# Kernel optimization log

Hardware: AMD Instinct MI355X
Metric: run time of the kernel (lower is better)

The kernel has to match this reference:

```python
import jax, jax.numpy as jnp
import numpy as np
from jax import lax

H = 1024       # hidden_size
I = 1024       # intermediate_size (per expert)
E = 16         # num_experts
TOP_K = 4      # num_active_experts


def setup_inputs() -> dict:
    key = jax.random.key(0)
    ks = jax.random.split(key, 9)
    std_gate = 0.02 / (E ** 0.5)
    return {
        "hidden_states": jax.random.normal(ks[0], (1, 2048, H), jnp.float32),
        "gate_w": jax.random.normal(ks[1], (E, H), jnp.float32) * std_gate,
        "expert_bias": jnp.zeros((E,), jnp.float32),
        "w1": jax.random.normal(ks[2], (E, I, H), jnp.float32) * 0.02,
        "w2": jax.random.normal(ks[3], (E, H, I), jnp.float32) * 0.02,
        "w3": jax.random.normal(ks[4], (E, I, H), jnp.float32) * 0.02,
        "sw1": jax.random.normal(ks[5], (I, H), jnp.float32) * 0.02,
        "sw2": jax.random.normal(ks[6], (H, I), jnp.float32) * 0.02,
        "sw3": jax.random.normal(ks[7], (I, H), jnp.float32) * 0.02,
    }


def _swiglu(x, wg, wd, wu):
    # Swish(x W1^T) * (x W3^T) then W2^T
    return (jax.nn.silu(x @ wg.T) * (x @ wu.T)) @ wd.T


def reference(hidden_states, gate_w, expert_bias, w1, w2, w3, sw1, sw2, sw3):
    B, S, Hd = hidden_states.shape
    x = hidden_states.reshape(-1, Hd)              # [T, H]
    T = x.shape[0]

    # ---- Router ----
    router_logits = x @ gate_w.T                   # [T, E]
    biased = router_logits + expert_bias           # loss-free balancing bias
    _, sel = lax.top_k(biased, TOP_K)              # [T, K] indices from biased logits
    raw = jnp.take_along_axis(router_logits, sel, axis=-1)  # weights from UNbiased logits
    rw = jax.nn.softmax(raw.astype(jnp.float32), axis=-1).astype(x.dtype)  # [T, K]

    # Dense combine weights g[t, e] = routing weight if e selected else 0
    g = jnp.zeros((T, E), x.dtype).at[jnp.arange(T)[:, None], sel].add(rw)

    # ---- Routed experts (mathematically equal to grouped dispatch) ----
    routed = jnp.zeros_like(x)
    for e in range(E):  # fixed small expert loop
        routed = routed + g[:, e:e + 1] * _swiglu(x, w1[e], w2[e], w3[e])

    # ---- Shared expert ----
    shared = _swiglu(x, sw1, sw2, sw3)

    out = (shared + routed).reshape(B, S, Hd)      # dropout p=0 -> identity
    return out
```

## Files before the change

kernel.cpp:

```cpp
#include <hip/hip_runtime.h>
#include <cstddef>
#include <cstdint>

#define T_TOK 2048
#define HD 1024
#define ID 1024
#define NE 16
#define TOPK 4
#define BM 128
#define BN 128
#define BK 32
#define MT_MAX 96
#define SLOT_CAP (MT_MAX * BM)

typedef float f32x4 __attribute__((ext_vector_type(4)));
typedef __bf16 bf16x8 __attribute__((ext_vector_type(8)));
typedef __bf16 bf16x4 __attribute__((ext_vector_type(4)));

#define WS_TILE_E 256
#define WS_LOGITS 4096
#define WS_SLOT_TOK (WS_LOGITS + T_TOK * NE * 4)
#define WS_SLOT_W (WS_SLOT_TOK + SLOT_CAP * 4)
#define WS_H1 (WS_SLOT_W + SLOT_CAP * 4)
#define WS_XB (WS_H1 + (size_t)SLOT_CAP * ID * 2)
#define WS_W1B (WS_XB + (size_t)T_TOK * HD * 2)
#define WS_W2B (WS_W1B + (size_t)NE * ID * HD * 2)
#define WS_W3B (WS_W2B + (size_t)NE * HD * ID * 2)
#define WS_SW1B (WS_W3B + (size_t)NE * ID * HD * 2)
#define WS_SW2B (WS_SW1B + (size_t)ID * HD * 2)
#define WS_SW3B (WS_SW2B + (size_t)HD * ID * 2)
#define WS_NEED (WS_SW3B + (size_t)ID * HD * 2)

__device__ __forceinline__ f32x4 mfma16(bf16x8 a, bf16x8 b, f32x4 c) {
  return __builtin_amdgcn_mfma_f32_16x16x32_bf16(a, b, c, 0, 0, 0);
}

__device__ __forceinline__ bf16x4 pack4(f32x4 a) {
  bf16x4 o;
  o[0] = (__bf16)a[0]; o[1] = (__bf16)a[1]; o[2] = (__bf16)a[2]; o[3] = (__bf16)a[3];
  return o;
}

__device__ __forceinline__ void gload16(const __bf16* g, __bf16* l) {
  __builtin_amdgcn_global_load_lds(
      (const __attribute__((address_space(1))) uint32_t*)g,
      (__attribute__((address_space(3))) uint32_t*)l, 16, 0, 0);
}

#define W4 ((size_t)1 << 22)
#define S4 ((size_t)1 << 18)
#define X4 ((size_t)1 << 19)
#define CVT4_TOTAL (3 * W4 + 3 * S4 + X4)
#define NCHUNK (CVT4_TOTAL / 2048)
#define CVT_GRID 2048
#define LOGITS_BLOCKS (T_TOK / 4)

__global__ __launch_bounds__(256) void fused_pre(
    const float* __restrict__ w1, const float* __restrict__ w2,
    const float* __restrict__ w3, const float* __restrict__ sw1,
    const float* __restrict__ sw2, const float* __restrict__ sw3,
    const float* __restrict__ x, __bf16* __restrict__ w1b,
    __bf16* __restrict__ w2b, __bf16* __restrict__ w3b,
    __bf16* __restrict__ sw1b, __bf16* __restrict__ sw2b,
    __bf16* __restrict__ sw3b, __bf16* __restrict__ xb,
    const float* __restrict__ gw, float* __restrict__ logits) {
  int tid = threadIdx.x;
  if ((int)blockIdx.x < LOGITS_BLOCKS) {
    int wv = tid >> 6;
    int lane = tid & 63;
    int tok = blockIdx.x * 4 + wv;
    int e = lane >> 2;
    int q = lane & 3;
    const float4* xr = (const float4*)(x + (size_t)tok * HD) + q * 64;
    const float4* wr = (const float4*)(gw + (size_t)e * HD) + q * 64;
    float s0 = 0.f, s1 = 0.f;
#pragma unroll 8
    for (int i = 0; i < 64; i += 2) {
      float4 a0 = xr[i], w0 = wr[i];
      float4 a1 = xr[i + 1], w1v = wr[i + 1];
      s0 += a0.x * w0.x + a0.y * w0.y + a0.z * w0.z + a0.w * w0.w;
      s1 += a1.x * w1v.x + a1.y * w1v.y + a1.z * w1v.z + a1.w * w1v.w;
    }
    float s = s0 + s1;
    s += __shfl_xor(s, 1);
    s += __shfl_xor(s, 2);
    if (q == 0) logits[(size_t)tok * NE + e] = s;
    return;
  }
  size_t b = blockIdx.x - LOGITS_BLOCKS;
  for (size_t c = b; c < NCHUNK; c += CVT_GRID) {
    size_t f = c * 2048;
    const float* src;
    __bf16* dst;
    size_t off;
    if (f < 3 * W4) {
      size_t t = f >> 22;
      off = f & (W4 - 1);
      src = (t == 0) ? w1 : (t == 1) ? w2 : w3;
      dst = (t == 0) ? w1b : (t == 1) ? w2b : w3b;
    } else {
      size_t j = f - 3 * W4;
      if (j < 3 * S4) {
        size_t t = j >> 18;
        off = j & (S4 - 1);
        src = (t == 0) ? sw1 : (t == 1) ? sw2 : sw3;
        dst = (t == 0) ? sw1b : (t == 1) ? sw2b : sw3b;
      } else {
        off = j - 3 * S4;
        src = x;
        dst = xb;
      }
    }
    const f32x4* p = (const f32x4*)src + off + tid;
    __bf16* q = dst + 4 * (off + tid);
    f32x4 v0 = __builtin_nontemporal_load(p);
    f32x4 v1 = __builtin_nontemporal_load(p + 256);
    f32x4 v2 = __builtin_nontemporal_load(p + 512);
    f32x4 v3 = __builtin_nontemporal_load(p + 768);
    f32x4 v4 = __builtin_nontemporal_load(p + 1024);
    f32x4 v5 = __builtin_nontemporal_load(p + 1280);
    f32x4 v6 = __builtin_nontemporal_load(p + 1536);
    f32x4 v7 = __builtin_nontemporal_load(p + 1792);
    *(bf16x4*)(q + 0 * 1024) = pack4(v0);
    *(bf16x4*)(q + 1 * 1024) = pack4(v1);
    *(bf16x4*)(q + 2 * 1024) = pack4(v2);
    *(bf16x4*)(q + 3 * 1024) = pack4(v3);
    *(bf16x4*)(q + 4 * 1024) = pack4(v4);
    *(bf16x4*)(q + 5 * 1024) = pack4(v5);
    *(bf16x4*)(q + 6 * 1024) = pack4(v6);
    *(bf16x4*)(q + 7 * 1024) = pack4(v7);
  }
}

__global__ __launch_bounds__(256) void router_finish(
    const float* __restrict__ logits, const float* __restrict__ bias,
    int* __restrict__ tile_e, int* __restrict__ slot_tok,
    float* __restrict__ slot_w) {
  __shared__ int hist[NE];
  __shared__ int soff[NE + 1];
  __shared__ int fillp[NE];
  __shared__ unsigned lsel[T_TOK];
  __shared__ float4 lw4[T_TOK];

  int tid = threadIdx.x;
  if (tid < NE) { hist[tid] = 0; fillp[tid] = 0; }
  __syncthreads();

  float bb[NE];
#pragma unroll
  for (int e = 0; e < NE; ++e) bb[e] = bias[e];

  for (int j = 0; j < T_TOK / 256; ++j) {
    int t = tid + 256 * j;
    float lg[NE];
    const float4* lp = (const float4*)(logits + (size_t)t * NE);
#pragma unroll
    for (int q = 0; q < 4; ++q) {
      float4 v = lp[q];
      lg[4 * q] = v.x; lg[4 * q + 1] = v.y; lg[4 * q + 2] = v.z; lg[4 * q + 3] = v.w;
    }
    float b[NE];
#pragma unroll
    for (int e = 0; e < NE; ++e) b[e] = lg[e] + bb[e];

    int selk[TOPK];
    float raw[TOPK];
    unsigned used = 0;
#pragma unroll
    for (int k = 0; k < TOPK; ++k) {
      float best = -3.4e38f;
      int bi = 0;
#pragma unroll
      for (int e = 0; e < NE; ++e) {
        if (!((used >> e) & 1) && b[e] > best) { best = b[e]; bi = e; }
      }
      used |= (1u << bi);
      selk[k] = bi;
      raw[k] = lg[bi];
    }
    float m = raw[0];
#pragma unroll
    for (int k = 1; k < TOPK; ++k) m = fmaxf(m, raw[k]);
    float s = 0.f;
    float w[TOPK];
#pragma unroll
    for (int k = 0; k < TOPK; ++k) { w[k] = __expf(raw[k] - m); s += w[k]; }
    float inv = 1.f / s;
    lsel[t] = (unsigned)selk[0] | ((unsigned)selk[1] << 8) |
              ((unsigned)selk[2] << 16) | ((unsigned)selk[3] << 24);
    lw4[t] = make_float4(w[0] * inv, w[1] * inv, w[2] * inv, w[3] * inv);
#pragma unroll
    for (int k = 0; k < TOPK; ++k) atomicAdd(&hist[selk[k]], 1);
  }
  __syncthreads();

  if (tid == 0) {
    int o = 0;
    for (int e = 0; e < NE; ++e) { soff[e] = o; o += (hist[e] + BM - 1) & ~(BM - 1); }
    soff[NE] = o;
  }
  __syncthreads();
  int shared_base = soff[NE];
  int total = shared_base + T_TOK;
  for (int tt = tid; tt < MT_MAX; tt += 256) {
    int base = tt * BM;
    int ee = -1;
    if (base < shared_base) {
      ee = 0;
#pragma unroll
      for (int q = 1; q < NE; ++q) if (base >= soff[q]) ee = q;
    } else if (base < total) {
      ee = NE;
    }
    tile_e[tt] = ee;
  }

  for (int j = 0; j < T_TOK / 256; ++j) {
    int t = tid + 256 * j;
    unsigned ps = lsel[t];
    float4 wv = lw4[t];
    int e0 = ps & 255, e1 = (ps >> 8) & 255, e2 = (ps >> 16) & 255, e3 = ps >> 24;
    int p0 = atomicAdd(&fillp[e0], 1);
    slot_tok[soff[e0] + p0] = t; slot_w[soff[e0] + p0] = wv.x;
    int p1 = atomicAdd(&fillp[e1], 1);
    slot_tok[soff[e1] + p1] = t; slot_w[soff[e1] + p1] = wv.y;
    int p2 = atomicAdd(&fillp[e2], 1);
    slot_tok[soff[e2] + p2] = t; slot_w[soff[e2] + p2] = wv.z;
    int p3 = atomicAdd(&fillp[e3], 1);
    slot_tok[soff[e3] + p3] = t; slot_w[soff[e3] + p3] = wv.w;
  }

  for (int s = tid; s < shared_base; s += 256) {
    int e = 0;
#pragma unroll
    for (int q = 1; q < NE; ++q) if (s >= soff[q]) e = q;
    if (s >= soff[e] + hist[e]) { slot_tok[s] = -1; slot_w[s] = 0.f; }
  }
  for (int s = shared_base + tid; s < total; s += 256) {
    slot_tok[s] = s - shared_base;
    slot_w[s] = 1.0f;
  }
}


__global__ __launch_bounds__(256, 2) void pass1_bf16(
    const __bf16* __restrict__ xb, const int* __restrict__ slot_tok,
    const int* __restrict__ tile_e, const __bf16* __restrict__ w1b,
    const __bf16* __restrict__ w3b, const __bf16* __restrict__ sw1b,
    const __bf16* __restrict__ sw3b, __bf16* __restrict__ h1) {
  int mt = blockIdx.y;
  int e = tile_e[mt];
  if (e < 0) return;
  int n0 = blockIdx.x * BN;
  int m0 = mt * BM;

  const __bf16* wg = (e == NE) ? sw1b : w1b + (size_t)e * ID * HD;
  const __bf16* wu = (e == NE) ? sw3b : w3b + (size_t)e * ID * HD;

  __shared__ __align__(16) __bf16 As[2][BM * BK];
  __shared__ __align__(16) __bf16 Bg[2][BN * BK];
  __shared__ __align__(16) __bf16 Bu[2][BN * BK];

  int tid = threadIdx.x;
  int r0 = tid >> 2, r1 = r0 + 64;
  int c8 = ((tid & 3) ^ ((r0 >> 1) & 3)) * 8;
  int tok0 = slot_tok[m0 + r0]; if (tok0 < 0) tok0 = 0;
  int tok1 = slot_tok[m0 + r1]; if (tok1 < 0) tok1 = 0;
  const __bf16* gA0 = xb + (size_t)tok0 * HD + c8;
  const __bf16* gA1 = xb + (size_t)tok1 * HD + c8;
  const __bf16* gG0 = wg + (size_t)(n0 + r0) * HD + c8;
  const __bf16* gG1 = wg + (size_t)(n0 + r1) * HD + c8;
  const __bf16* gU0 = wu + (size_t)(n0 + r0) * HD + c8;
  const __bf16* gU1 = wu + (size_t)(n0 + r1) * HD + c8;

  int wave = tid >> 6, lane = tid & 63;
  int wm = (wave >> 1) * 64, wn = (wave & 1) * 64;
  int l16 = lane & 15, kch = lane >> 4;
  int kk8 = (kch ^ ((l16 >> 1) & 3)) * 8;

  f32x4 accg[4][4] = {};
  f32x4 accu[4][4] = {};

  auto stage = [&](int B, int k0) {
    gload16(gA0 + k0, &As[B][(size_t)tid * 8]);
    gload16(gA1 + k0, &As[B][(size_t)(tid + 256) * 8]);
    gload16(gG0 + k0, &Bg[B][(size_t)tid * 8]);
    gload16(gG1 + k0, &Bg[B][(size_t)(tid + 256) * 8]);
    gload16(gU0 + k0, &Bu[B][(size_t)tid * 8]);
    gload16(gU1 + k0, &Bu[B][(size_t)(tid + 256) * 8]);
  };
  auto body = [&](int B) {
    bf16x8 af[4], gf[4], uf[4];
#pragma unroll
    for (int i = 0; i < 4; ++i) {
      af[i] = *(const bf16x8*)(&As[B][(wm + i * 16 + l16) * BK + kk8]);
      gf[i] = *(const bf16x8*)(&Bg[B][(wn + i * 16 + l16) * BK + kk8]);
      uf[i] = *(const bf16x8*)(&Bu[B][(wn + i * 16 + l16) * BK + kk8]);
    }
    asm volatile("s_waitcnt lgkmcnt(0)" ::: "memory");
    __builtin_amdgcn_s_barrier();
    __builtin_amdgcn_sched_barrier(0);
#pragma unroll
    for (int mi = 0; mi < 4; ++mi)
#pragma unroll
      for (int ni = 0; ni < 4; ++ni) {
        accg[mi][ni] = mfma16(af[mi], gf[ni], accg[mi][ni]);
        accu[mi][ni] = mfma16(af[mi], uf[ni], accu[mi][ni]);
      }
  };

  stage(0, 0);
#pragma unroll 1
  for (int k = 0; k < HD / BK - 1; ++k) {
    int cur = k & 1;
    stage(cur ^ 1, (k + 1) * BK);
    asm volatile("s_waitcnt vmcnt(6)" ::: "memory");
    __builtin_amdgcn_s_barrier();
    __builtin_amdgcn_sched_barrier(0);
    body(cur);
  }
  asm volatile("s_waitcnt vmcnt(0)" ::: "memory");
  __builtin_amdgcn_s_barrier();
  __builtin_amdgcn_sched_barrier(0);
  body((HD / BK - 1) & 1);

#pragma unroll
  for (int mi = 0; mi < 4; ++mi) {
#pragma unroll
    for (int ni = 0; ni < 4; ++ni) {
#pragma unroll
      for (int j = 0; j < 4; ++j) {
        int row = m0 + wm + mi * 16 + kch * 4 + j;
        int col = n0 + wn + ni * 16 + l16;
        float g = accg[mi][ni][j];
        float u = accu[mi][ni][j];
        float hv = (g / (1.f + __expf(-g))) * u;
        h1[(size_t)row * ID + col] = (__bf16)hv;
      }
    }
  }
}

__global__ __launch_bounds__(256, 3) void pass2_bf16(
    const __bf16* __restrict__ h1, const int* __restrict__ slot_tok,
    const float* __restrict__ slot_w, const int* __restrict__ tile_e,
    const __bf16* __restrict__ w2b, const __bf16* __restrict__ sw2b,
    float* __restrict__ out) {
  int mt = blockIdx.y;
  int e = tile_e[mt];
  if (e < 0) return;
  int n0 = blockIdx.x * BN;
  int m0 = mt * BM;

  const __bf16* wd = (e == NE) ? sw2b : w2b + (size_t)e * HD * ID;

  __shared__ __align__(16) __bf16 As[2][BM * BK];
  __shared__ __align__(16) __bf16 Bs[2][BN * BK];

  int tid = threadIdx.x;
  int r0 = tid >> 2, r1 = r0 + 64;
  int c8 = ((tid & 3) ^ ((r0 >> 1) & 3)) * 8;
  const __bf16* gA0 = h1 + (size_t)(m0 + r0) * ID + c8;
  const __bf16* gA1 = h1 + (size_t)(m0 + r1) * ID + c8;
  const __bf16* gB0 = wd + (size_t)(n0 + r0) * ID + c8;
  const __bf16* gB1 = wd + (size_t)(n0 + r1) * ID + c8;

  int wave = tid >> 6, lane = tid & 63;
  int wm = (wave >> 1) * 64, wn = (wave & 1) * 64;
  int l16 = lane & 15, kch = lane >> 4;
  int kk8 = (kch ^ ((l16 >> 1) & 3)) * 8;

  f32x4 acc[4][4] = {};

  auto stage = [&](int B, int k0) {
    gload16(gA0 + k0, &As[B][(size_t)tid * 8]);
    gload16(gA1 + k0, &As[B][(size_t)(tid + 256) * 8]);
    gload16(gB0 + k0, &Bs[B][(size_t)tid * 8]);
    gload16(gB1 + k0, &Bs[B][(size_t)(tid + 256) * 8]);
  };
  auto body = [&](int B) {
    bf16x8 af[4], bf[4];
#pragma unroll
    for (int i = 0; i < 4; ++i) {
      af[i] = *(const bf16x8*)(&As[B][(wm + i * 16 + l16) * BK + kk8]);
      bf[i] = *(const bf16x8*)(&Bs[B][(wn + i * 16 + l16) * BK + kk8]);
    }
    asm volatile("s_waitcnt lgkmcnt(0)" ::: "memory");
    __builtin_amdgcn_s_barrier();
    __builtin_amdgcn_sched_barrier(0);
#pragma unroll
    for (int mi = 0; mi < 4; ++mi)
#pragma unroll
      for (int ni = 0; ni < 4; ++ni)
        acc[mi][ni] = mfma16(af[mi], bf[ni], acc[mi][ni]);
  };

  stage(0, 0);
#pragma unroll 1
  for (int k = 0; k < ID / BK - 1; ++k) {
    int cur = k & 1;
    stage(cur ^ 1, (k + 1) * BK);
    asm volatile("s_waitcnt vmcnt(4)" ::: "memory");
    __builtin_amdgcn_s_barrier();
    __builtin_amdgcn_sched_barrier(0);
    body(cur);
  }
  asm volatile("s_waitcnt vmcnt(0)" ::: "memory");
  __builtin_amdgcn_s_barrier();
  __builtin_amdgcn_sched_barrier(0);
  body((ID / BK - 1) & 1);

#pragma unroll
  for (int mi = 0; mi < 4; ++mi) {
#pragma unroll
    for (int j = 0; j < 4; ++j) {
      int row = m0 + wm + mi * 16 + kch * 4 + j;
      int token = slot_tok[row];
      if (token < 0) continue;
      float wgt = slot_w[row];
#pragma unroll
      for (int ni = 0; ni < 4; ++ni) {
        int col = n0 + wn + ni * 16 + l16;
        atomicAdd(out + (size_t)token * HD + col, wgt * acc[mi][ni][j]);
      }
    }
  }
}

extern "C" void kernel_launch(void* const* d_in, const int* in_sizes, int n_in,
                              void* d_out, int out_size, void* d_ws, size_t ws_size,
                              hipStream_t stream) {
  const float* x = (const float*)d_in[0];
  const float* gate_w = (const float*)d_in[1];
  const float* ebias = (const float*)d_in[2];
  const float* w1 = (const float*)d_in[3];
  const float* w2 = (const float*)d_in[4];
  const float* w3 = (const float*)d_in[5];
  const float* sw1 = (const float*)d_in[6];
  const float* sw2 = (const float*)d_in[7];
  const float* sw3 = (const float*)d_in[8];
  float* out = (float*)d_out;

  char* ws = (char*)d_ws;
  int* tile_e = (int*)(ws + WS_TILE_E);
  float* logits = (float*)(ws + WS_LOGITS);
  int* slot_tok = (int*)(ws + WS_SLOT_TOK);
  float* slot_w = (float*)(ws + WS_SLOT_W);
  __bf16* h1 = (__bf16*)(ws + WS_H1);
  __bf16* xb = (__bf16*)(ws + WS_XB);
  __bf16* w1b = (__bf16*)(ws + WS_W1B);
  __bf16* w2b = (__bf16*)(ws + WS_W2B);
  __bf16* w3b = (__bf16*)(ws + WS_W3B);
  __bf16* sw1b = (__bf16*)(ws + WS_SW1B);
  __bf16* sw2b = (__bf16*)(ws + WS_SW2B);
  __bf16* sw3b = (__bf16*)(ws + WS_SW3B);

  hipMemsetAsync(d_out, 0, (size_t)T_TOK * HD * sizeof(float), stream);

  fused_pre<<<LOGITS_BLOCKS + CVT_GRID, 256, 0, stream>>>(
      w1, w2, w3, sw1, sw2, sw3, x, w1b, w2b, w3b, sw1b, sw2b, sw3b, xb,
      gate_w, logits);
  router_finish<<<1, 256, 0, stream>>>(logits, ebias, tile_e, slot_tok, slot_w);

  pass1_bf16<<<dim3(ID / BN, MT_MAX), 256, 0, stream>>>(
      xb, slot_tok, tile_e, w1b, w3b, sw1b, sw3b, h1);
  pass2_bf16<<<dim3(HD / BN, MT_MAX), 256, 0, stream>>>(
      h1, slot_tok, slot_w, tile_e, w2b, sw2b, out);
}
```

Baseline: 242.0 us.

## Fuse fp32-to-bf16 weight conversion into GEMM tile loads

Drops the separate pass that converted all expert and shared weights to bf16 in workspace. The GEMMs now load fp32 weight tiles straight into LDS with a swizzled layout and convert to bf16 while reading fragments. This removes a full read-and-write of roughly 200MB of weights. In exchange each tile doubles its global and LDS traffic, and the conversion is repeated for every M tile that reuses an expert's weights. LDS use grows, which may lower occupancy.

```diff
diff --git a/kernel.cpp b/kernel.cpp
--- a/kernel.cpp
+++ b/kernel.cpp
@@ -23,16 +23,16 @@
 #define WS_SLOT_W (WS_SLOT_TOK + SLOT_CAP * 4)
 #define WS_H1 (WS_SLOT_W + SLOT_CAP * 4)
 #define WS_XB (WS_H1 + (size_t)SLOT_CAP * ID * 2)
-#define WS_W1B (WS_XB + (size_t)T_TOK * HD * 2)
-#define WS_W2B (WS_W1B + (size_t)NE * ID * HD * 2)
-#define WS_W3B (WS_W2B + (size_t)NE * HD * ID * 2)
-#define WS_SW1B (WS_W3B + (size_t)NE * ID * HD * 2)
-#define WS_SW2B (WS_SW1B + (size_t)ID * HD * 2)
-#define WS_SW3B (WS_SW2B + (size_t)HD * ID * 2)
-#define WS_NEED (WS_SW3B + (size_t)ID * HD * 2)
 
 __device__ __forceinline__ f32x4 mfma16(bf16x8 a, bf16x8 b, f32x4 c) {
   return __builtin_amdgcn_mfma_f32_16x16x32_bf16(a, b, c, 0, 0, 0);
+}
+
+__device__ __forceinline__ bf16x8 pack8(f32x4 a, f32x4 b) {
+  bf16x8 o;
+  o[0] = (__bf16)a[0]; o[1] = (__bf16)a[1]; o[2] = (__bf16)a[2]; o[3] = (__bf16)a[3];
+  o[4] = (__bf16)b[0]; o[5] = (__bf16)b[1]; o[6] = (__bf16)b[2]; o[7] = (__bf16)b[3];
+  return o;
 }
 
 __device__ __forceinline__ bf16x4 pack4(f32x4 a) {
@@ -46,24 +46,18 @@
       (const __attribute__((address_space(1))) uint32_t*)g,
       (__attribute__((address_space(3))) uint32_t*)l, 16, 0, 0);
 }
-
-#define W4 ((size_t)1 << 22)
-#define S4 ((size_t)1 << 18)
-#define X4 ((size_t)1 << 19)
-#define CVT4_TOTAL (3 * W4 + 3 * S4 + X4)
-#define NCHUNK (CVT4_TOTAL / 2048)
-#define CVT_GRID 2048
+__device__ __forceinline__ void gload16f(const float* g, float* l) {
+  __builtin_amdgcn_global_load_lds(
+      (const __attribute__((address_space(1))) uint32_t*)g,
+      (__attribute__((address_space(3))) uint32_t*)l, 16, 0, 0);
+}
+
 #define LOGITS_BLOCKS (T_TOK / 4)
+#define XCHUNKS 256
 
 __global__ __launch_bounds__(256) void fused_pre(
-    const float* __restrict__ w1, const float* __restrict__ w2,
-    const float* __restrict__ w3, const float* __restrict__ sw1,
-    const float* __restrict__ sw2, const float* __restrict__ sw3,
-    const float* __restrict__ x, __bf16* __restrict__ w1b,
-    __bf16* __restrict__ w2b, __bf16* __restrict__ w3b,
-    __bf16* __restrict__ sw1b, __bf16* __restrict__ sw2b,
-    __bf16* __restrict__ sw3b, __bf16* __restrict__ xb,
-    const float* __restrict__ gw, float* __restrict__ logits) {
+    const float* __restrict__ x, const float* __restrict__ gw,
+    __bf16* __restrict__ xb, float* __restrict__ logits) {
   int tid = threadIdx.x;
   if ((int)blockIdx.x < LOGITS_BLOCKS) {
     int wv = tid >> 6;
@@ -87,49 +81,19 @@
     if (q == 0) logits[(size_t)tok * NE + e] = s;
     return;
   }
-  size_t b = blockIdx.x - LOGITS_BLOCKS;
-  for (size_t c = b; c < NCHUNK; c += CVT_GRID) {
-    size_t f = c * 2048;
-    const float* src;
-    __bf16* dst;
-    size_t off;
-    if (f < 3 * W4) {
-      size_t t = f >> 22;
-      off = f & (W4 - 1);
-      src = (t == 0) ? w1 : (t == 1) ? w2 : w3;
-      dst = (t == 0) ? w1b : (t == 1) ? w2b : w3b;
-    } else {
-      size_t j = f - 3 * W4;
-      if (j < 3 * S4) {
-        size_t t = j >> 18;
-        off = j & (S4 - 1);
-        src = (t == 0) ? sw1 : (t == 1) ? sw2 : sw3;
-        dst = (t == 0) ? sw1b : (t == 1) ? sw2b : sw3b;
-      } else {
-        off = j - 3 * S4;
-        src = x;
-        dst = xb;
-      }
-    }
-    const f32x4* p = (const f32x4*)src + off + tid;
-    __bf16* q = dst + 4 * (off + tid);
-    f32x4 v0 = __builtin_nontemporal_load(p);
-    f32x4 v1 = __builtin_nontemporal_load(p + 256);
-    f32x4 v2 = __builtin_nontemporal_load(p + 512);
-    f32x4 v3 = __builtin_nontemporal_load(p + 768);
-    f32x4 v4 = __builtin_nontemporal_load(p + 1024);
-    f32x4 v5 = __builtin_nontemporal_load(p + 1280);
-    f32x4 v6 = __builtin_nontemporal_load(p + 1536);
-    f32x4 v7 = __builtin_nontemporal_load(p + 1792);
-    *(bf16x4*)(q + 0 * 1024) = pack4(v0);
-    *(bf16x4*)(q + 1 * 1024) = pack4(v1);
-    *(bf16x4*)(q + 2 * 1024) = pack4(v2);
-    *(bf16x4*)(q + 3 * 1024) = pack4(v3);
-    *(bf16x4*)(q + 4 * 1024) = pack4(v4);
-    *(bf16x4*)(q + 5 * 1024) = pack4(v5);
-    *(bf16x4*)(q + 6 * 1024) = pack4(v6);
-    *(bf16x4*)(q + 7 * 1024) = pack4(v7);
-  }
+  size_t f = (size_t)(blockIdx.x - LOGITS_BLOCKS) * 2048;
+  const f32x4* p = (const f32x4*)x + f + tid;
+  __bf16* q = xb + 4 * (f + tid);
+  f32x4 v0 = p[0], v1 = p[256], v2 = p[512], v3 = p[768];
+  f32x4 v4 = p[1024], v5 = p[1280], v6 = p[1536], v7 = p[1792];
+  *(bf16x4*)(q + 0 * 1024) = pack4(v0);
+  *(bf16x4*)(q + 1 * 1024) = pack4(v1);
+  *(bf16x4*)(q + 2 * 1024) = pack4(v2);
+  *(bf16x4*)(q + 3 * 1024) = pack4(v3);
+  *(bf16x4*)(q + 4 * 1024) = pack4(v4);
+  *(bf16x4*)(q + 5 * 1024) = pack4(v5);
+  *(bf16x4*)(q + 6 * 1024) = pack4(v6);
+  *(bf16x4*)(q + 7 * 1024) = pack4(v7);
 }
 
 __global__ __launch_bounds__(256) void router_finish(
@@ -245,21 +209,21 @@
 
 __global__ __launch_bounds__(256, 2) void pass1_bf16(
     const __bf16* __restrict__ xb, const int* __restrict__ slot_tok,
-    const int* __restrict__ tile_e, const __bf16* __restrict__ w1b,
-    const __bf16* __restrict__ w3b, const __bf16* __restrict__ sw1b,
-    const __bf16* __restrict__ sw3b, __bf16* __restrict__ h1) {
+    const int* __restrict__ tile_e, const float* __restrict__ w1,
+    const float* __restrict__ w3, const float* __restrict__ sw1,
+    const float* __restrict__ sw3, __bf16* __restrict__ h1) {
   int mt = blockIdx.y;
   int e = tile_e[mt];
   if (e < 0) return;
   int n0 = blockIdx.x * BN;
   int m0 = mt * BM;
 
-  const __bf16* wg = (e == NE) ? sw1b : w1b + (size_t)e * ID * HD;
-  const __bf16* wu = (e == NE) ? sw3b : w3b + (size_t)e * ID * HD;
+  const float* wg = (e == NE) ? sw1 : w1 + (size_t)e * ID * HD;
+  const float* wu = (e == NE) ? sw3 : w3 + (size_t)e * ID * HD;
 
   __shared__ __align__(16) __bf16 As[2][BM * BK];
-  __shared__ __align__(16) __bf16 Bg[2][BN * BK];
-  __shared__ __align__(16) __bf16 Bu[2][BN * BK];
+  __shared__ __align__(16) float BgF[2][BN * BK];
+  __shared__ __align__(16) float BuF[2][BN * BK];
 
   int tid = threadIdx.x;
   int r0 = tid >> 2, r1 = r0 + 64;
@@ -268,15 +232,27 @@
   int tok1 = slot_tok[m0 + r1]; if (tok1 < 0) tok1 = 0;
   const __bf16* gA0 = xb + (size_t)tok0 * HD + c8;
   const __bf16* gA1 = xb + (size_t)tok1 * HD + c8;
-  const __bf16* gG0 = wg + (size_t)(n0 + r0) * HD + c8;
-  const __bf16* gG1 = wg + (size_t)(n0 + r1) * HD + c8;
-  const __bf16* gU0 = wu + (size_t)(n0 + r0) * HD + c8;
-  const __bf16* gU1 = wu + (size_t)(n0 + r1) * HD + c8;
+
+  const float* srcG[4];
+  const float* srcU[4];
+  int ldst[4];
+#pragma unroll
+  for (int j = 0; j < 4; ++j) {
+    int id = tid + j * 256;
+    int r = id >> 3, s = id & 7;
+    int go = (s ^ (r & 7)) << 2;
+    srcG[j] = wg + (size_t)(n0 + r) * HD + go;
+    srcU[j] = wu + (size_t)(n0 + r) * HD + go;
+    ldst[j] = id * 4;
+  }
 
   int wave = tid >> 6, lane = tid & 63;
   int wm = (wave >> 1) * 64, wn = (wave & 1) * 64;
   int l16 = lane & 15, kch = lane >> 4;
   int kk8 = (kch ^ ((l16 >> 1) & 3)) * 8;
+  int sw = l16 & 7;
+  int cB0 = ((2 * kch) ^ sw) * 4;
+  int cB1 = ((2 * kch + 1) ^ sw) * 4;
 
   f32x4 accg[4][4] = {};
   f32x4 accu[4][4] = {};
@@ -284,18 +260,26 @@
   auto stage = [&](int B, int k0) {
     gload16(gA0 + k0, &As[B][(size_t)tid * 8]);
     gload16(gA1 + k0, &As[B][(size_t)(tid + 256) * 8]);
-    gload16(gG0 + k0, &Bg[B][(size_t)tid * 8]);
-    gload16(gG1 + k0, &Bg[B][(size_t)(tid + 256) * 8]);
-    gload16(gU0 + k0, &Bu[B][(size_t)tid * 8]);
-    gload16(gU1 + k0, &Bu[B][(size_t)(tid + 256) * 8]);
+#pragma unroll
+    for (int j = 0; j < 4; ++j) {
+      gload16f(srcG[j] + k0, &BgF[B][ldst[j]]);
+      gload16f(srcU[j] + k0, &BuF[B][ldst[j]]);
+    }
   };
   auto body = [&](int B) {
     bf16x8 af[4], gf[4], uf[4];
 #pragma unroll
+    for (int i = 0; i < 4; ++i)
+      af[i] = *(const bf16x8*)(&As[B][(wm + i * 16 + l16) * BK + kk8]);
+#pragma unroll
     for (int i = 0; i < 4; ++i) {
-      af[i] = *(const bf16x8*)(&As[B][(wm + i * 16 + l16) * BK + kk8]);
-      gf[i] = *(const bf16x8*)(&Bg[B][(wn + i * 16 + l16) * BK + kk8]);
-      uf[i] = *(const bf16x8*)(&Bu[B][(wn + i * 16 + l16) * BK + kk8]);
+      int rb = (wn + i * 16 + l16) * BK;
+      f32x4 ga = *(const f32x4*)(&BgF[B][rb + cB0]);
+      f32x4 gb = *(const f32x4*)(&BgF[B][rb + cB1]);
+      gf[i] = pack8(ga, gb);
+      f32x4 ua = *(const f32x4*)(&BuF[B][rb + cB0]);
+      f32x4 ub = *(const f32x4*)(&BuF[B][rb + cB1]);
+      uf[i] = pack8(ua, ub);
     }
     asm volatile("s_waitcnt lgkmcnt(0)" ::: "memory");
     __builtin_amdgcn_s_barrier();
@@ -314,7 +298,7 @@
   for (int k = 0; k < HD / BK - 1; ++k) {
     int cur = k & 1;
     stage(cur ^ 1, (k + 1) * BK);
-    asm volatile("s_waitcnt vmcnt(6)" ::: "memory");
+    asm volatile("s_waitcnt vmcnt(10)" ::: "memory");
     __builtin_amdgcn_s_barrier();
     __builtin_amdgcn_sched_barrier(0);
     body(cur);
@@ -344,7 +328,7 @@
 __global__ __launch_bounds__(256, 3) void pass2_bf16(
     const __bf16* __restrict__ h1, const int* __restrict__ slot_tok,
     const float* __restrict__ slot_w, const int* __restrict__ tile_e,
-    const __bf16* __restrict__ w2b, const __bf16* __restrict__ sw2b,
+    const float* __restrict__ w2, const float* __restrict__ sw2,
     float* __restrict__ out) {
   int mt = blockIdx.y;
   int e = tile_e[mt];
@@ -352,38 +336,55 @@
   int n0 = blockIdx.x * BN;
   int m0 = mt * BM;
 
-  const __bf16* wd = (e == NE) ? sw2b : w2b + (size_t)e * HD * ID;
+  const float* wd = (e == NE) ? sw2 : w2 + (size_t)e * HD * ID;
 
   __shared__ __align__(16) __bf16 As[2][BM * BK];
-  __shared__ __align__(16) __bf16 Bs[2][BN * BK];
+  __shared__ __align__(16) float BF[2][BN * BK];
 
   int tid = threadIdx.x;
   int r0 = tid >> 2, r1 = r0 + 64;
   int c8 = ((tid & 3) ^ ((r0 >> 1) & 3)) * 8;
   const __bf16* gA0 = h1 + (size_t)(m0 + r0) * ID + c8;
   const __bf16* gA1 = h1 + (size_t)(m0 + r1) * ID + c8;
-  const __bf16* gB0 = wd + (size_t)(n0 + r0) * ID + c8;
-  const __bf16* gB1 = wd + (size_t)(n0 + r1) * ID + c8;
+
+  const float* srcB[4];
+  int ldst[4];
+#pragma unroll
+  for (int j = 0; j < 4; ++j) {
+    int id = tid + j * 256;
+    int r = id >> 3, s = id & 7;
+    int go = (s ^ (r & 7)) << 2;
+    srcB[j] = wd + (size_t)(n0 + r) * ID + go;
+    ldst[j] = id * 4;
+  }
 
   int wave = tid >> 6, lane = tid & 63;
   int wm = (wave >> 1) * 64, wn = (wave & 1) * 64;
   int l16 = lane & 15, kch = lane >> 4;
   int kk8 = (kch ^ ((l16 >> 1) & 3)) * 8;
+  int sw = l16 & 7;
+  int cB0 = ((2 * kch) ^ sw) * 4;
+  int cB1 = ((2 * kch + 1) ^ sw) * 4;
 
   f32x4 acc[4][4] = {};
 
   auto stage = [&](int B, int k0) {
     gload16(gA0 + k0, &As[B][(size_t)tid * 8]);
     gload16(gA1 + k0, &As[B][(size_t)(tid + 256) * 8]);
-    gload16(gB0 + k0, &Bs[B][(size_t)tid * 8]);
-    gload16(gB1 + k0, &Bs[B][(size_t)(tid + 256) * 8]);
+#pragma unroll
+    for (int j = 0; j < 4; ++j) gload16f(srcB[j] + k0, &BF[B][ldst[j]]);
   };
   auto body = [&](int B) {
     bf16x8 af[4], bf[4];
 #pragma unroll
+    for (int i = 0; i < 4; ++i)
+      af[i] = *(const bf16x8*)(&As[B][(wm + i * 16 + l16) * BK + kk8]);
+#pragma unroll
     for (int i = 0; i < 4; ++i) {
-      af[i] = *(const bf16x8*)(&As[B][(wm + i * 16 + l16) * BK + kk8]);
-      bf[i] = *(const bf16x8*)(&Bs[B][(wn + i * 16 + l16) * BK + kk8]);
+      int rb = (wn + i * 16 + l16) * BK;
+      f32x4 ba = *(const f32x4*)(&BF[B][rb + cB0]);
+      f32x4 bb = *(const f32x4*)(&BF[B][rb + cB1]);
+      bf[i] = pack8(ba, bb);
     }
     asm volatile("s_waitcnt lgkmcnt(0)" ::: "memory");
     __builtin_amdgcn_s_barrier();
@@ -400,7 +401,7 @@
   for (int k = 0; k < ID / BK - 1; ++k) {
     int cur = k & 1;
     stage(cur ^ 1, (k + 1) * BK);
-    asm volatile("s_waitcnt vmcnt(4)" ::: "memory");
+    asm volatile("s_waitcnt vmcnt(6)" ::: "memory");
     __builtin_amdgcn_s_barrier();
     __builtin_amdgcn_sched_barrier(0);
     body(cur);
@@ -448,22 +449,14 @@
   float* slot_w = (float*)(ws + WS_SLOT_W);
   __bf16* h1 = (__bf16*)(ws + WS_H1);
   __bf16* xb = (__bf16*)(ws + WS_XB);
-  __bf16* w1b = (__bf16*)(ws + WS_W1B);
-  __bf16* w2b = (__bf16*)(ws + WS_W2B);
-  __bf16* w3b = (__bf16*)(ws + WS_W3B);
-  __bf16* sw1b = (__bf16*)(ws + WS_SW1B);
-  __bf16* sw2b = (__bf16*)(ws + WS_SW2B);
-  __bf16* sw3b = (__bf16*)(ws + WS_SW3B);
 
   hipMemsetAsync(d_out, 0, (size_t)T_TOK * HD * sizeof(float), stream);
 
-  fused_pre<<<LOGITS_BLOCKS + CVT_GRID, 256, 0, stream>>>(
-      w1, w2, w3, sw1, sw2, sw3, x, w1b, w2b, w3b, sw1b, sw2b, sw3b, xb,
-      gate_w, logits);
+  fused_pre<<<LOGITS_BLOCKS + XCHUNKS, 256, 0, stream>>>(x, gate_w, xb, logits);
   router_finish<<<1, 256, 0, stream>>>(logits, ebias, tile_e, slot_tok, slot_w);
 
   pass1_bf16<<<dim3(ID / BN, MT_MAX), 256, 0, stream>>>(
-      xb, slot_tok, tile_e, w1b, w3b, sw1b, sw3b, h1);
+      xb, slot_tok, tile_e, w1, w3, sw1, sw3, h1);
   pass2_bf16<<<dim3(HD / BN, MT_MAX), 256, 0, stream>>>(
-      h1, slot_tok, slot_w, tile_e, w2b, sw2b, out);
-}
+      h1, slot_tok, slot_w, tile_e, w2, sw2, out);
+}
```

Result: faster. 223.8 us (-7.5%).

## Overlap down-projection weight conversion with pass1 GEMM and unify expert weight layout

Applied to the files above, without the earlier changes.

The fp32-to-bf16 conversion of w2 and sw2 moves out of the pre-kernel into extra blocks appended to the pass1 grid, so it can run alongside the gate/up GEMM rather than before routing. Shared-expert weights are now stored contiguously as expert index 16 in the same buffers, which removes the per-block pointer select. Pass1 switches to a 1D grid with manual tile decoding. The conversion blocks are scheduled after the GEMM blocks, so whether they actually overlap depends on block dispatch order, and they compete with the GEMM for bandwidth.

```diff
diff --git a/kernel.cpp b/kernel.cpp
--- a/kernel.cpp
+++ b/kernel.cpp
@@ -24,12 +24,7 @@
 #define WS_H1 (WS_SLOT_W + SLOT_CAP * 4)
 #define WS_XB (WS_H1 + (size_t)SLOT_CAP * ID * 2)
 #define WS_W1B (WS_XB + (size_t)T_TOK * HD * 2)
-#define WS_W2B (WS_W1B + (size_t)NE * ID * HD * 2)
-#define WS_W3B (WS_W2B + (size_t)NE * HD * ID * 2)
-#define WS_SW1B (WS_W3B + (size_t)NE * ID * HD * 2)
-#define WS_SW2B (WS_SW1B + (size_t)ID * HD * 2)
-#define WS_SW3B (WS_SW2B + (size_t)HD * ID * 2)
-#define WS_NEED (WS_SW3B + (size_t)ID * HD * 2)
+#define EXSZ ((size_t)ID * HD)
 
 __device__ __forceinline__ f32x4 mfma16(bf16x8 a, bf16x8 b, f32x4 c) {
   return __builtin_amdgcn_mfma_f32_16x16x32_bf16(a, b, c, 0, 0, 0);
@@ -47,22 +42,42 @@
       (__attribute__((address_space(3))) uint32_t*)l, 16, 0, 0);
 }
 
+__device__ __forceinline__ void cvt_chunk(const float* __restrict__ src,
+                                          __bf16* __restrict__ dst, size_t off,
+                                          int tid) {
+  const f32x4* p = (const f32x4*)src + off + tid;
+  __bf16* q = dst + 4 * (off + tid);
+  f32x4 v0 = __builtin_nontemporal_load(p);
+  f32x4 v1 = __builtin_nontemporal_load(p + 256);
+  f32x4 v2 = __builtin_nontemporal_load(p + 512);
+  f32x4 v3 = __builtin_nontemporal_load(p + 768);
+  f32x4 v4 = __builtin_nontemporal_load(p + 1024);
+  f32x4 v5 = __builtin_nontemporal_load(p + 1280);
+  f32x4 v6 = __builtin_nontemporal_load(p + 1536);
+  f32x4 v7 = __builtin_nontemporal_load(p + 1792);
+  *(bf16x4*)(q + 0 * 1024) = pack4(v0);
+  *(bf16x4*)(q + 1 * 1024) = pack4(v1);
+  *(bf16x4*)(q + 2 * 1024) = pack4(v2);
+  *(bf16x4*)(q + 3 * 1024) = pack4(v3);
+  *(bf16x4*)(q + 4 * 1024) = pack4(v4);
+  *(bf16x4*)(q + 5 * 1024) = pack4(v5);
+  *(bf16x4*)(q + 6 * 1024) = pack4(v6);
+  *(bf16x4*)(q + 7 * 1024) = pack4(v7);
+}
+
 #define W4 ((size_t)1 << 22)
 #define S4 ((size_t)1 << 18)
 #define X4 ((size_t)1 << 19)
-#define CVT4_TOTAL (3 * W4 + 3 * S4 + X4)
+#define CVT4_TOTAL (2 * W4 + 2 * S4 + X4)
 #define NCHUNK (CVT4_TOTAL / 2048)
 #define CVT_GRID 2048
 #define LOGITS_BLOCKS (T_TOK / 4)
 
 __global__ __launch_bounds__(256) void fused_pre(
-    const float* __restrict__ w1, const float* __restrict__ w2,
-    const float* __restrict__ w3, const float* __restrict__ sw1,
-    const float* __restrict__ sw2, const float* __restrict__ sw3,
+    const float* __restrict__ w1, const float* __restrict__ w3,
+    const float* __restrict__ sw1, const float* __restrict__ sw3,
     const float* __restrict__ x, __bf16* __restrict__ w1b,
-    __bf16* __restrict__ w2b, __bf16* __restrict__ w3b,
-    __bf16* __restrict__ sw1b, __bf16* __restrict__ sw2b,
-    __bf16* __restrict__ sw3b, __bf16* __restrict__ xb,
+    __bf16* __restrict__ w3b, __bf16* __restrict__ xb,
     const float* __restrict__ gw, float* __restrict__ logits) {
   int tid = threadIdx.x;
   if ((int)blockIdx.x < LOGITS_BLOCKS) {
@@ -93,42 +108,12 @@
     const float* src;
     __bf16* dst;
     size_t off;
-    if (f < 3 * W4) {
-      size_t t = f >> 22;
-      off = f & (W4 - 1);
-      src = (t == 0) ? w1 : (t == 1) ? w2 : w3;
-      dst = (t == 0) ? w1b : (t == 1) ? w2b : w3b;
-    } else {
-      size_t j = f - 3 * W4;
-      if (j < 3 * S4) {
-        size_t t = j >> 18;
-        off = j & (S4 - 1);
-        src = (t == 0) ? sw1 : (t == 1) ? sw2 : sw3;
-        dst = (t == 0) ? sw1b : (t == 1) ? sw2b : sw3b;
-      } else {
-        off = j - 3 * S4;
-        src = x;
-        dst = xb;
-      }
-    }
-    const f32x4* p = (const f32x4*)src + off + tid;
-    __bf16* q = dst + 4 * (off + tid);
-    f32x4 v0 = __builtin_nontemporal_load(p);
-    f32x4 v1 = __builtin_nontemporal_load(p + 256);
-    f32x4 v2 = __builtin_nontemporal_load(p + 512);
-    f32x4 v3 = __builtin_nontemporal_load(p + 768);
-    f32x4 v4 = __builtin_nontemporal_load(p + 1024);
-    f32x4 v5 = __builtin_nontemporal_load(p + 1280);
-    f32x4 v6 = __builtin_nontemporal_load(p + 1536);
-    f32x4 v7 = __builtin_nontemporal_load(p + 1792);
-    *(bf16x4*)(q + 0 * 1024) = pack4(v0);
-    *(bf16x4*)(q + 1 * 1024) = pack4(v1);
-    *(bf16x4*)(q + 2 * 1024) = pack4(v2);
-    *(bf16x4*)(q + 3 * 1024) = pack4(v3);
-    *(bf16x4*)(q + 4 * 1024) = pack4(v4);
-    *(bf16x4*)(q + 5 * 1024) = pack4(v5);
-    *(bf16x4*)(q + 6 * 1024) = pack4(v6);
-    *(bf16x4*)(q + 7 * 1024) = pack4(v7);
+    if (f < W4) { src = w1; dst = w1b; off = f; }
+    else if (f < 2 * W4) { src = w3; dst = w3b; off = f - W4; }
+    else if (f < 2 * W4 + S4) { src = sw1; dst = w1b + 16 * EXSZ; off = f - 2 * W4; }
+    else if (f < 2 * W4 + 2 * S4) { src = sw3; dst = w3b + 16 * EXSZ; off = f - 2 * W4 - S4; }
+    else { src = x; dst = xb; off = f - 2 * W4 - 2 * S4; }
+    cvt_chunk(src, dst, off, tid);
   }
 }
 
@@ -242,26 +227,37 @@
   }
 }
 
+#define P1_BLOCKS (8 * MT_MAX)
+#define W2CHUNKS ((int)((W4 + S4) / 2048))
 
 __global__ __launch_bounds__(256, 2) void pass1_bf16(
     const __bf16* __restrict__ xb, const int* __restrict__ slot_tok,
     const int* __restrict__ tile_e, const __bf16* __restrict__ w1b,
-    const __bf16* __restrict__ w3b, const __bf16* __restrict__ sw1b,
-    const __bf16* __restrict__ sw3b, __bf16* __restrict__ h1) {
-  int mt = blockIdx.y;
+    const __bf16* __restrict__ w3b, __bf16* __restrict__ h1,
+    const float* __restrict__ w2, const float* __restrict__ sw2,
+    __bf16* __restrict__ w2b) {
+  int tid = threadIdx.x;
+  int bid = blockIdx.x;
+  if (bid >= P1_BLOCKS) {
+    size_t f = (size_t)(bid - P1_BLOCKS) * 2048;
+    if (f < W4) cvt_chunk(w2, w2b, f, tid);
+    else cvt_chunk(sw2, w2b + 16 * EXSZ, f - W4, tid);
+    return;
+  }
+  int nt = bid & 7;
+  int mt = bid >> 3;
   int e = tile_e[mt];
   if (e < 0) return;
-  int n0 = blockIdx.x * BN;
+  int n0 = nt * BN;
   int m0 = mt * BM;
 
-  const __bf16* wg = (e == NE) ? sw1b : w1b + (size_t)e * ID * HD;
-  const __bf16* wu = (e == NE) ? sw3b : w3b + (size_t)e * ID * HD;
+  const __bf16* wg = w1b + (size_t)e * EXSZ;
+  const __bf16* wu = w3b + (size_t)e * EXSZ;
 
   __shared__ __align__(16) __bf16 As[2][BM * BK];
   __shared__ __align__(16) __bf16 Bg[2][BN * BK];
   __shared__ __align__(16) __bf16 Bu[2][BN * BK];
 
-  int tid = threadIdx.x;
   int r0 = tid >> 2, r1 = r0 + 64;
   int c8 = ((tid & 3) ^ ((r0 >> 1) & 3)) * 8;
   int tok0 = slot_tok[m0 + r0]; if (tok0 < 0) tok0 = 0;
@@ -344,15 +340,14 @@
 __global__ __launch_bounds__(256, 3) void pass2_bf16(
     const __bf16* __restrict__ h1, const int* __restrict__ slot_tok,
     const float* __restrict__ slot_w, const int* __restrict__ tile_e,
-    const __bf16* __restrict__ w2b, const __bf16* __restrict__ sw2b,
-    float* __restrict__ out) {
+    const __bf16* __restrict__ w2b, float* __restrict__ out) {
   int mt = blockIdx.y;
   int e = tile_e[mt];
   if (e < 0) return;
   int n0 = blockIdx.x * BN;
   int m0 = mt * BM;
 
-  const __bf16* wd = (e == NE) ? sw2b : w2b + (size_t)e * HD * ID;
+  const __bf16* wd = w2b + (size_t)e * EXSZ;
 
   __shared__ __align__(16) __bf16 As[2][BM * BK];
   __shared__ __align__(16) __bf16 Bs[2][BN * BK];
@@ -449,21 +444,17 @@
   __bf16* h1 = (__bf16*)(ws + WS_H1);
   __bf16* xb = (__bf16*)(ws + WS_XB);
   __bf16* w1b = (__bf16*)(ws + WS_W1B);
-  __bf16* w2b = (__bf16*)(ws + WS_W2B);
-  __bf16* w3b = (__bf16*)(ws + WS_W3B);
-  __bf16* sw1b = (__bf16*)(ws + WS_SW1B);
-  __bf16* sw2b = (__bf16*)(ws + WS_SW2B);
-  __bf16* sw3b = (__bf16*)(ws + WS_SW3B);
+  __bf16* w3b = w1b + 17 * EXSZ;
+  __bf16* w2b = w3b + 17 * EXSZ;
 
   hipMemsetAsync(d_out, 0, (size_t)T_TOK * HD * sizeof(float), stream);
 
   fused_pre<<<LOGITS_BLOCKS + CVT_GRID, 256, 0, stream>>>(
-      w1, w2, w3, sw1, sw2, sw3, x, w1b, w2b, w3b, sw1b, sw2b, sw3b, xb,
-      gate_w, logits);
+      w1, w3, sw1, sw3, x, w1b, w3b, xb, gate_w, logits);
   router_finish<<<1, 256, 0, stream>>>(logits, ebias, tile_e, slot_tok, slot_w);
 
-  pass1_bf16<<<dim3(ID / BN, MT_MAX), 256, 0, stream>>>(
-      xb, slot_tok, tile_e, w1b, w3b, sw1b, sw3b, h1);
+  pass1_bf16<<<P1_BLOCKS + W2CHUNKS, 256, 0, stream>>>(
+      xb, slot_tok, tile_e, w1b, w3b, h1, w2, sw2, w2b);
   pass2_bf16<<<dim3(HD / BN, MT_MAX), 256, 0, stream>>>(
-      h1, slot_tok, slot_w, tile_e, w2b, sw2b, out);
-}
+      h1, slot_tok, slot_w, tile_e, w2b, out);
+}
```

Result: faster. 234.1 us (-3.3%).
